# Performance work log

Measured on AMD Instinct MI355X. Metric: run time of the kernel, lower is better.

The kernel has to match this reference:

```python
import jax, jax.numpy as jnp
import numpy as np

H = 32  # hidden_layer_size

def setup_inputs() -> dict:
    key = jax.random.key(0)
    ks = jax.random.split(key, 12)
    B, T, I = 4096, 512, 1
    x = jax.random.normal(ks[0], (B, T, I), dtype=jnp.float32)
    # linear_1: input_size -> H
    W1 = jax.random.normal(ks[1], (H, I), dtype=jnp.float32) * (1.0 / np.sqrt(I))
    b1 = jnp.zeros((H,), dtype=jnp.float32)
    # LSTM layer 0 (input H) and layer 1 (input H); torch gate order i,f,g,o
    Wih0 = jax.random.normal(ks[2], (4 * H, H), dtype=jnp.float32) * np.sqrt(2.0 / H)  # kaiming
    Whh0 = jax.random.normal(ks[3], (4 * H, H), dtype=jnp.float32) * (1.0 / np.sqrt(H))
    bih0 = jnp.zeros((4 * H,), dtype=jnp.float32)
    bhh0 = jnp.zeros((4 * H,), dtype=jnp.float32)
    Wih1 = jax.random.normal(ks[4], (4 * H, H), dtype=jnp.float32) * np.sqrt(2.0 / H)
    Whh1 = jax.random.normal(ks[5], (4 * H, H), dtype=jnp.float32) * (1.0 / np.sqrt(H))
    bih1 = jnp.zeros((4 * H,), dtype=jnp.float32)
    bhh1 = jnp.zeros((4 * H,), dtype=jnp.float32)
    # linear_2: num_layers*H -> 1
    W2 = jax.random.normal(ks[6], (1, 2 * H), dtype=jnp.float32) * (1.0 / np.sqrt(2 * H))
    b2 = jnp.zeros((1,), dtype=jnp.float32)
    return {"x": x, "W1": W1, "b1": b1,
            "Wih0": Wih0, "Whh0": Whh0, "bih0": bih0, "bhh0": bhh0,
            "Wih1": Wih1, "Whh1": Whh1, "bih1": bih1, "bhh1": bhh1,
            "W2": W2, "b2": b2}


def _lstm_layer(inp, Wih, Whh, bih, bhh):
    # inp: [B, T, H_in]; returns (ys [B, T, H], h_final [B, H])
    B = inp.shape[0]
    # precompute input-to-gate projections for all timesteps (one big GEMM)
    pre = jnp.einsum('bti,gi->tbg', inp, Wih) + (bih + bhh)  # [T, B, 4H]

    def step(carry, p_t):
        h, c = carry
        z = p_t + h @ Whh.T  # [B, 4H]
        i, f, g, o = jnp.split(z, 4, axis=-1)
        i = jax.nn.sigmoid(i)
        f = jax.nn.sigmoid(f)
        g = jnp.tanh(g)
        o = jax.nn.sigmoid(o)
        c = f * c + i * g
        h = o * jnp.tanh(c)
        return (h, c), h

    h0 = jnp.zeros((B, H), dtype=inp.dtype)
    c0 = jnp.zeros((B, H), dtype=inp.dtype)
    (h_f, _), ys = jax.lax.scan(step, (h0, c0), pre)
    return jnp.transpose(ys, (1, 0, 2)), h_f


def reference(x, W1, b1, Wih0, Whh0, bih0, bhh0, Wih1, Whh1, bih1, bhh1, W2, b2):
    # linear_1 + ReLU
    h = jax.nn.relu(jnp.einsum('bti,oi->bto', x, W1) + b1)  # [B, T, H]
    y0, hf0 = _lstm_layer(h, Wih0, Whh0, bih0, bhh0)
    _, hf1 = _lstm_layer(y0, Wih1, Whh1, bih1, bhh1)
    # h_n.permute(1,0,2).reshape(B, -1) -> concat layer finals along feature dim
    hcat = jnp.concatenate([hf0, hf1], axis=-1)  # [B, 2H]
    # dropout: eval mode (identity)
    preds = hcat @ W2.T + b2  # [B, 1]
    return preds[:, -1]  # [B]
```

## Files before the change

### kernel.cpp

```cpp
#include <hip/hip_runtime.h>

#define HH 32
#define NB 16
#define NT 512
#define TT 512

typedef float f32x4 __attribute__((ext_vector_type(4)));
typedef __bf16 bf16x8 __attribute__((ext_vector_type(8)));
typedef unsigned int u32;
typedef unsigned short u16;
typedef u32 u32x4 __attribute__((ext_vector_type(4)));

#if __has_builtin(__builtin_amdgcn_exp2f)
#define EXP2F(x) __builtin_amdgcn_exp2f(x)
#else
#define EXP2F(x) exp2f(x)
#endif
#if __has_builtin(__builtin_amdgcn_rcpf)
#define RCPF(x) __builtin_amdgcn_rcpf(x)
#else
#define RCPF(x) (1.0f / (x))
#endif

static __device__ __forceinline__ float sigm(float z) {
  return RCPF(1.0f + EXP2F(z * -1.44269504f));
}
static __device__ __forceinline__ float tanh_fast(float z) {
  return __builtin_fmaf(2.0f, RCPF(1.0f + EXP2F(z * -2.88539008f)), -1.0f);
}
static __device__ __forceinline__ f32x4 mfma16(bf16x8 a, bf16x8 b, f32x4 c) {
  return __builtin_amdgcn_mfma_f32_16x16x32_bf16(a, b, c, 0, 0, 0);
}

static __device__ __forceinline__ u32 rne_hi(u32 b) {
  return (b + 0x7FFFu + ((b >> 16) & 1u)) & 0xFFFF0000u;
}
static __device__ __forceinline__ u32 pack_hi16(u32 a, u32 b) {
#if __has_builtin(__builtin_amdgcn_perm)
  return __builtin_amdgcn_perm(a, b, 0x03020706u);
#else
  return (b & 0xFFFF0000u) | (a >> 16);
#endif
}
static __device__ __forceinline__ void split8(const float f[8], bf16x8* hi, bf16x8* lo) {
  u32 r[8];
  float lof[8];
#pragma unroll
  for (int j = 0; j < 8; ++j) {
    u32 b = __builtin_bit_cast(u32, f[j]);
    r[j] = rne_hi(b);
    lof[j] = f[j] - __builtin_bit_cast(float, r[j]);
  }
  u32x4 hw, lw;
#pragma unroll
  for (int i = 0; i < 4; ++i) {
    hw[i] = pack_hi16(r[2 * i], r[2 * i + 1]);
    lw[i] = pack_hi16(__builtin_bit_cast(u32, lof[2 * i]),
                      __builtin_bit_cast(u32, lof[2 * i + 1]));
  }
  *hi = __builtin_bit_cast(bf16x8, hw);
  *lo = __builtin_bit_cast(bf16x8, lw);
}

static __device__ __forceinline__ void load_wfrag(const float* __restrict__ M,
                                                  int tile, int lane,
                                                  bf16x8* hi, bf16x8* lo) {
  const int m = lane & 15;
  const int gi = (m & 3) * HH + 4 * tile + (m >> 2);
  const int k0 = (lane >> 4) * 8;
  const float* p = M + gi * HH + k0;
  float f[8];
#pragma unroll
  for (int e = 0; e < 8; ++e) f[e] = p[e];
  split8(f, hi, lo);
}

static __device__ __forceinline__ void store_h(u16* hiA, u16* loA, int fw, float h) {
  const u32 b = __builtin_bit_cast(u32, h);
  const u32 r = rne_hi(b);
  hiA[fw] = (u16)(r >> 16);
  const float lof = h - __builtin_bit_cast(float, r);
  loA[fw] = (u16)(__builtin_bit_cast(u32, lof) >> 16);
}

__global__ void __launch_bounds__(NT)
lstm_fused_v3(const float* __restrict__ x,
              const float* __restrict__ W1, const float* __restrict__ b1,
              const float* __restrict__ Wih0, const float* __restrict__ Whh0,
              const float* __restrict__ bih0, const float* __restrict__ bhh0,
              const float* __restrict__ Wih1, const float* __restrict__ Whh1,
              const float* __restrict__ bih1, const float* __restrict__ bhh1,
              const float* __restrict__ W2, const float* __restrict__ b2,
              float* __restrict__ out, int T)
{
  __shared__ __align__(16) u16 h0hi[2][NB * HH], h0lo[2][NB * HH];
  __shared__ __align__(16) u16 h1hi[2][NB * HH], h1lo[2][NB * HH];
  __shared__ __align__(16) u16 hxhi[2][NB * HH], hxlo[2][NB * HH];
  __shared__ __align__(16) float xT[TT * NB];

  const int tid  = threadIdx.x;
  const int w    = tid >> 6;
  const int lane = tid & 63;
  const int ub   = lane & 15;
  const int G    = lane >> 4;
  const int uu   = 4 * w + G;
  const int b0   = blockIdx.x * NB;

  bf16x8 whh0h, whh0l, wih0h, wih0l, wih1h, wih1l, whh1h, whh1l;
  load_wfrag(Whh0, w, lane, &whh0h, &whh0l);
  load_wfrag(Wih0, w, lane, &wih0h, &wih0l);
  load_wfrag(Wih1, w, lane, &wih1h, &wih1l);
  load_wfrag(Whh1, w, lane, &whh1h, &whh1l);

  f32x4 B0c, B1c;
#pragma unroll
  for (int q = 0; q < 4; ++q) {
    B0c[q] = bih0[q * HH + uu] + bhh0[q * HH + uu];
    B1c[q] = bih1[q * HH + uu] + bhh1[q * HH + uu];
  }
  const float W1u = W1[uu];
  const float b1u = b1[uu];

  const int fw  = (ub + ((uu >> 3) << 4)) * 8 + (uu & 7);
  const int frd = lane * 8;

  {
    const int row = tid >> 5;
    const int c0i = (tid & 31) * 16;
    if (c0i + 16 <= T) {
      const float* xp = x + (size_t)(b0 + row) * T + c0i;
#pragma unroll
      for (int j = 0; j < 16; j += 4) {
        float4 v = *(const float4*)(xp + j);
        xT[(c0i + j + 0) * NB + row] = v.x;
        xT[(c0i + j + 1) * NB + row] = v.y;
        xT[(c0i + j + 2) * NB + row] = v.z;
        xT[(c0i + j + 3) * NB + row] = v.w;
      }
    }
  }
  h0hi[0][tid] = 0; h0hi[1][tid] = 0; h0lo[0][tid] = 0; h0lo[1][tid] = 0;
  h1hi[0][tid] = 0; h1hi[1][tid] = 0; h1lo[0][tid] = 0; h1lo[1][tid] = 0;
  {
    const float hv = fmaxf(__builtin_fmaf(x[(size_t)(b0 + ub) * T], W1u, b1u), 0.0f);
    const u32 bb = __builtin_bit_cast(u32, hv);
    const u32 rr = rne_hi(bb);
    hxhi[0][fw] = (u16)(rr >> 16);
    const float lf = hv - __builtin_bit_cast(float, rr);
    hxlo[0][fw] = (u16)(__builtin_bit_cast(u32, lf) >> 16);
  }
  float c0 = 0.0f, c1 = 0.0f, h0v = 0.0f, h1v = 0.0f;
  __syncthreads();

#define STEP(kk, WB, DO_L0, DO_L1, DO_HIN)                                   \
  {                                                                          \
    const int RB = (WB) ^ 1;                                                 \
    const bf16x8 a0h = *(const bf16x8*)&h0hi[RB][frd];                       \
    const bf16x8 a0l = *(const bf16x8*)&h0lo[RB][frd];                       \
    bf16x8 a1h, a1l, axh, axl;                                               \
    if (DO_L1) { a1h = *(const bf16x8*)&h1hi[WB][frd];                       \
                 a1l = *(const bf16x8*)&h1lo[WB][frd]; }                     \
    if (DO_L0) { axh = *(const bf16x8*)&hxhi[WB][frd];                       \
                 axl = *(const bf16x8*)&hxlo[WB][frd]; }                     \
    if (DO_HIN) {        \
      const float xv = xT[((kk) + 1) * NB + ub];                             \
      const float hv = fmaxf(__builtin_fmaf(xv, W1u, b1u), 0.0f);            \
      const u32 bb = __builtin_bit_cast(u32, hv);                            \
      const u32 rr = rne_hi(bb);                                             \
      hxhi[RB][fw] = (u16)(rr >> 16);                                        \
      const float lf = hv - __builtin_bit_cast(float, rr);                   \
      hxlo[RB][fw] = (u16)(__builtin_bit_cast(u32, lf) >> 16);               \
    }                                                                        \
    if (DO_L0) {                                                             \
      f32x4 z = B0c;                                                         \
      z = mfma16(whh0h, a0h, z); z = mfma16(whh0h, a0l, z);                  \
      z = mfma16(whh0l, a0h, z);                                             \
      z = mfma16(wih0h, axh, z); z = mfma16(wih0h, axl, z);                  \
      z = mfma16(wih0l, axh, z);                                             \
      const float iv = sigm(z[0]), fv = sigm(z[1]);                          \
      const float gv = tanh_fast(z[2]), ov = sigm(z[3]);                     \
      c0 = __builtin_fmaf(fv, c0, iv * gv);                                  \
      h0v = ov * tanh_fast(c0);                                              \
      store_h(h0hi[WB], h0lo[WB], fw, h0v);                                  \
    }                                                                        \
    if (DO_L1) {                                                             \
      f32x4 z = B1c;                                                         \
      z = mfma16(whh1h, a1h, z); z = mfma16(whh1h, a1l, z);                  \
      z = mfma16(whh1l, a1h, z);                                             \
      z = mfma16(wih1h, a0h, z); z = mfma16(wih1h, a0l, z);                  \
      z = mfma16(wih1l, a0h, z);                                             \
      const float iv = sigm(z[0]), fv = sigm(z[1]);                          \
      const float gv = tanh_fast(z[2]), ov = sigm(z[3]);                     \
      c1 = __builtin_fmaf(fv, c1, iv * gv);                                  \
      h1v = ov * tanh_fast(c1);                                              \
      store_h(h1hi[RB], h1lo[RB], fw, h1v);                                  \
    }                                                                        \
    __syncthreads();                                                         \
  }

  STEP(0, 0, true, false, true);
  for (int kk = 1; kk + 1 < T; kk += 2) {
    STEP(kk, 1, true, true, true);
    STEP(kk + 1, 0, true, true, true);
  }
  STEP(T - 1, 1, true, true, false);
  STEP(T, 0, false, true, false);

#undef STEP

  xT[uu * NB + ub] = __builtin_fmaf(h0v, W2[uu], h1v * W2[HH + uu]);
  __syncthreads();
  if (tid < NB) {
    float acc = b2[0];
#pragma unroll
    for (int u = 0; u < HH; ++u) acc += xT[u * NB + tid];
    out[b0 + tid] = acc;
  }
}

extern "C" void kernel_launch(void* const* d_in, const int* in_sizes, int n_in,
                              void* d_out, int out_size, void* d_ws, size_t ws_size,
                              hipStream_t stream) {
  const float* x    = (const float*)d_in[0];
  const float* W1   = (const float*)d_in[1];
  const float* b1   = (const float*)d_in[2];
  const float* Wih0 = (const float*)d_in[3];
  const float* Whh0 = (const float*)d_in[4];
  const float* bih0 = (const float*)d_in[5];
  const float* bhh0 = (const float*)d_in[6];
  const float* Wih1 = (const float*)d_in[7];
  const float* Whh1 = (const float*)d_in[8];
  const float* bih1 = (const float*)d_in[9];
  const float* bhh1 = (const float*)d_in[10];
  const float* W2   = (const float*)d_in[11];
  const float* b2   = (const float*)d_in[12];

  const int B = out_size;
  const int I = in_sizes[1] / HH;
  const int T = in_sizes[0] / (B * I);
  const int blocks = B / NB;

  lstm_fused_v3<<<blocks, NT, 0, stream>>>(
      x, W1, b1, Wih0, Whh0, bih0, bhh0, Wih1, Whh1, bih1, bhh1, W2, b2,
      (float*)d_out, T);
}
```

Before: 262.9 us.

## Halve batch per block to 8 rows, doubling blocks and merging MFMA halves via DPP

New measurement: 410.2 us. 1.56x slower.

```diff
diff --git a/kernel.cpp b/kernel.cpp
--- a/kernel.cpp
+++ b/kernel.cpp
@@ -1,8 +1,8 @@
 #include <hip/hip_runtime.h>
 
 #define HH 32
-#define NB 16
-#define NT 512
+#define NB 8
+#define NT 256
 #define TT 512
 
 typedef float f32x4 __attribute__((ext_vector_type(4)));
@@ -22,14 +22,29 @@
 #define RCPF(x) (1.0f / (x))
 #endif
 
-static __device__ __forceinline__ float sigm(float z) {
-  return RCPF(1.0f + EXP2F(z * -1.44269504f));
-}
-static __device__ __forceinline__ float tanh_fast(float z) {
-  return __builtin_fmaf(2.0f, RCPF(1.0f + EXP2F(z * -2.88539008f)), -1.0f);
+#define S_SIGM (-1.44269504f)
+#define S_TANH (-2.88539008f)
+
+static __device__ __forceinline__ float sigm_pre(float zp) {
+  return RCPF(1.0f + EXP2F(zp));
+}
+static __device__ __forceinline__ float tanh_pre(float zp) {
+  return __builtin_fmaf(2.0f, RCPF(1.0f + EXP2F(zp)), -1.0f);
 }
 static __device__ __forceinline__ f32x4 mfma16(bf16x8 a, bf16x8 b, f32x4 c) {
   return __builtin_amdgcn_mfma_f32_16x16x32_bf16(a, b, c, 0, 0, 0);
+}
+
+static __device__ __forceinline__ float merge_dpp(float zA, float zB) {
+#if __has_builtin(__builtin_amdgcn_update_dpp)
+  return __builtin_bit_cast(float, __builtin_amdgcn_update_dpp(
+      __builtin_bit_cast(int, zA), __builtin_bit_cast(int, zB),
+      0x118 , 0xF , 0xC , false));
+#else
+  const int lane = threadIdx.x & 63;
+  const float mv = __shfl_up(zB, 8, 16);
+  return (lane & 8) ? mv : zA;
+#endif
 }
 
 static __device__ __forceinline__ u32 rne_hi(u32 b) {
@@ -62,16 +77,19 @@
   *lo = __builtin_bit_cast(bf16x8, lw);
 }
 
+
 static __device__ __forceinline__ void load_wfrag(const float* __restrict__ M,
                                                   int tile, int lane,
                                                   bf16x8* hi, bf16x8* lo) {
   const int m = lane & 15;
-  const int gi = (m & 3) * HH + 4 * tile + (m >> 2);
-  const int k0 = (lane >> 4) * 8;
-  const float* p = M + gi * HH + k0;
+  const int q = m & 3;
+  const int gi = q * HH + 4 * tile + (m >> 2);
+  const int kappa = lane >> 4;
+  const float s = (q == 2) ? S_TANH : S_SIGM;
   float f[8];
 #pragma unroll
-  for (int e = 0; e < 8; ++e) f[e] = p[e];
+  for (int e = 0; e < 8; ++e)
+    f[e] = M[gi * HH + 8 * kappa + 4 * (e & 1) + (e >> 1)] * s;
   split8(f, hi, lo);
 }
 
@@ -84,7 +102,7 @@
 }
 
 __global__ void __launch_bounds__(NT)
-lstm_fused_v3(const float* __restrict__ x,
+lstm_fused_v4(const float* __restrict__ x,
               const float* __restrict__ W1, const float* __restrict__ b1,
               const float* __restrict__ Wih0, const float* __restrict__ Whh0,
               const float* __restrict__ bih0, const float* __restrict__ bhh0,
@@ -93,36 +111,49 @@
               const float* __restrict__ W2, const float* __restrict__ b2,
               float* __restrict__ out, int T)
 {
-  __shared__ __align__(16) u16 h0hi[2][NB * HH], h0lo[2][NB * HH];
-  __shared__ __align__(16) u16 h1hi[2][NB * HH], h1lo[2][NB * HH];
-  __shared__ __align__(16) u16 hxhi[2][NB * HH], hxlo[2][NB * HH];
+  __shared__ __align__(16) u16 h0hi[2][16 * HH], h0lo[2][16 * HH];
+  __shared__ __align__(16) u16 h1hi[2][16 * HH], h1lo[2][16 * HH];
+  __shared__ __align__(16) u16 hxhi[2][16 * HH], hxlo[2][16 * HH];
   __shared__ __align__(16) float xT[TT * NB];
 
   const int tid  = threadIdx.x;
   const int w    = tid >> 6;
   const int lane = tid & 63;
-  const int ub   = lane & 15;
   const int G    = lane >> 4;
-  const int uu   = 4 * w + G;
   const int b0   = blockIdx.x * NB;
 
-  bf16x8 whh0h, whh0l, wih0h, wih0l, wih1h, wih1l, whh1h, whh1l;
-  load_wfrag(Whh0, w, lane, &whh0h, &whh0l);
-  load_wfrag(Wih0, w, lane, &wih0h, &wih0l);
-  load_wfrag(Wih1, w, lane, &wih1h, &wih1l);
-  load_wfrag(Whh1, w, lane, &whh1h, &whh1l);
-
-  f32x4 B0c, B1c;
-#pragma unroll
-  for (int q = 0; q < 4; ++q) {
-    B0c[q] = bih0[q * HH + uu] + bhh0[q * HH + uu];
-    B1c[q] = bih1[q * HH + uu] + bhh1[q * HH + uu];
-  }
-  const float W1u = W1[uu];
-  const float b1u = b1[uu];
-
-  const int fw  = (ub + ((uu >> 3) << 4)) * 8 + (uu & 7);
+  bf16x8 whh0hA, whh0lA, wih0hA, wih0lA, wih1hA, wih1lA, whh1hA, whh1lA;
+  bf16x8 whh0hB, whh0lB, wih0hB, wih0lB, wih1hB, wih1lB, whh1hB, whh1lB;
+  load_wfrag(Whh0, w,     lane, &whh0hA, &whh0lA);
+  load_wfrag(Wih0, w,     lane, &wih0hA, &wih0lA);
+  load_wfrag(Wih1, w,     lane, &wih1hA, &wih1lA);
+  load_wfrag(Whh1, w,     lane, &whh1hA, &whh1lA);
+  load_wfrag(Whh0, w + 4, lane, &whh0hB, &whh0lB);
+  load_wfrag(Wih0, w + 4, lane, &wih0hB, &wih0lB);
+  load_wfrag(Wih1, w + 4, lane, &wih1hB, &wih1lB);
+  load_wfrag(Whh1, w + 4, lane, &whh1hB, &whh1lB);
+
+  f32x4 bias0A, bias0B, bias1A, bias1B;
+  {
+    const int uA = 4 * w + G, uB = 4 * (w + 4) + G;
+#pragma unroll
+    for (int q = 0; q < 4; ++q) {
+      const float s = (q == 2) ? S_TANH : S_SIGM;
+      bias0A[q] = (bih0[q * HH + uA] + bhh0[q * HH + uA]) * s;
+      bias0B[q] = (bih0[q * HH + uB] + bhh0[q * HH + uB]) * s;
+      bias1A[q] = (bih1[q * HH + uA] + bhh1[q * HH + uA]) * s;
+      bias1B[q] = (bih1[q * HH + uB] + bhh1[q * HH + uB]) * s;
+    }
+  }
+  const f32x4 fzero = {0.f, 0.f, 0.f, 0.f};
+
+  const int bq = lane & 7;
+  const int uu = 4 * w + G + 16 * ((lane >> 3) & 1);
+  const int fw  = (bq + 16 * (uu >> 3)) * 8 + 2 * (uu & 3) + ((uu >> 2) & 1);
   const int frd = lane * 8;
+
+  const float W1u = W1[uu], b1u = b1[uu];
+  const float W2a = W2[uu], W2b = W2[HH + uu];
 
   {
     const int row = tid >> 5;
@@ -139,15 +170,20 @@
       }
     }
   }
-  h0hi[0][tid] = 0; h0hi[1][tid] = 0; h0lo[0][tid] = 0; h0lo[1][tid] = 0;
-  h1hi[0][tid] = 0; h1hi[1][tid] = 0; h1lo[0][tid] = 0; h1lo[1][tid] = 0;
   {
-    const float hv = fmaxf(__builtin_fmaf(x[(size_t)(b0 + ub) * T], W1u, b1u), 0.0f);
-    const u32 bb = __builtin_bit_cast(u32, hv);
-    const u32 rr = rne_hi(bb);
-    hxhi[0][fw] = (u16)(rr >> 16);
-    const float lf = hv - __builtin_bit_cast(float, rr);
-    hxlo[0][fw] = (u16)(__builtin_bit_cast(u32, lf) >> 16);
+    u32* z0 = (u32*)h0hi;
+    (void)z0;
+#pragma unroll
+    for (int j = 0; j < 2; ++j) {
+      ((u32*)h0hi[j])[tid] = 0; ((u32*)h0lo[j])[tid] = 0;
+      ((u32*)h1hi[j])[tid] = 0; ((u32*)h1lo[j])[tid] = 0;
+      ((u32*)hxhi[j])[tid] = 0; ((u32*)hxlo[j])[tid] = 0;
+    }
+  }
+  __syncthreads();
+  {
+    const float hv = fmaxf(__builtin_fmaf(x[(size_t)(b0 + bq) * T], W1u, b1u), 0.0f);
+    store_h(hxhi[0], hxlo[0], fw, hv);
   }
   float c0 = 0.0f, c1 = 0.0f, h0v = 0.0f, h1v = 0.0f;
   __syncthreads();
@@ -162,37 +198,55 @@
                  a1l = *(const bf16x8*)&h1lo[WB][frd]; }                     \
     if (DO_L0) { axh = *(const bf16x8*)&hxhi[WB][frd];                       \
                  axl = *(const bf16x8*)&hxlo[WB][frd]; }                     \
-    if (DO_HIN) {        \
-      const float xv = xT[((kk) + 1) * NB + ub];                             \
+    if (DO_HIN) {                 \
+      const float xv = xT[((kk) + 1) * NB + bq];                             \
       const float hv = fmaxf(__builtin_fmaf(xv, W1u, b1u), 0.0f);            \
-      const u32 bb = __builtin_bit_cast(u32, hv);                            \
-      const u32 rr = rne_hi(bb);                                             \
-      hxhi[RB][fw] = (u16)(rr >> 16);                                        \
-      const float lf = hv - __builtin_bit_cast(float, rr);                   \
-      hxlo[RB][fw] = (u16)(__builtin_bit_cast(u32, lf) >> 16);               \
+      store_h(hxhi[RB], hxlo[RB], fw, hv);                                   \
     }                                                                        \
     if (DO_L0) {                                                             \
-      f32x4 z = B0c;                                                         \
-      z = mfma16(whh0h, a0h, z); z = mfma16(whh0h, a0l, z);                  \
-      z = mfma16(whh0l, a0h, z);                                             \
-      z = mfma16(wih0h, axh, z); z = mfma16(wih0h, axl, z);                  \
-      z = mfma16(wih0l, axh, z);                                             \
-      const float iv = sigm(z[0]), fv = sigm(z[1]);                          \
-      const float gv = tanh_fast(z[2]), ov = sigm(z[3]);                     \
+      f32x4 rA = mfma16(whh0hA, a0h, bias0A);                                \
+      rA = mfma16(whh0hA, a0l, rA);                                          \
+      rA = mfma16(whh0lA, a0h, rA);                                          \
+      f32x4 iA = mfma16(wih0hA, axh, fzero);                                 \
+      iA = mfma16(wih0hA, axl, iA);                                          \
+      iA = mfma16(wih0lA, axh, iA);                                          \
+      f32x4 rB = mfma16(whh0hB, a0h, bias0B);                                \
+      rB = mfma16(whh0hB, a0l, rB);                                          \
+      rB = mfma16(whh0lB, a0h, rB);                                          \
+      f32x4 iB = mfma16(wih0hB, axh, fzero);                                 \
+      iB = mfma16(wih0hB, axl, iB);                                          \
+      iB = mfma16(wih0lB, axh, iB);                                          \
+      const f32x4 zA = rA + iA, zB = rB + iB;                                \
+      f32x4 zm;                                                              \
+      zm[0] = merge_dpp(zA[0], zB[0]); zm[1] = merge_dpp(zA[1], zB[1]);      \
+      zm[2] = merge_dpp(zA[2], zB[2]); zm[3] = merge_dpp(zA[3], zB[3]);      \
+      const float iv = sigm_pre(zm[0]), fv = sigm_pre(zm[1]);                \
+      const float gv = tanh_pre(zm[2]), ov = sigm_pre(zm[3]);                \
       c0 = __builtin_fmaf(fv, c0, iv * gv);                                  \
-      h0v = ov * tanh_fast(c0);                                              \
+      h0v = ov * tanh_pre(c0 * S_TANH);                                      \
       store_h(h0hi[WB], h0lo[WB], fw, h0v);                                  \
     }                                                                        \
     if (DO_L1) {                                                             \
-      f32x4 z = B1c;                                                         \
-      z = mfma16(whh1h, a1h, z); z = mfma16(whh1h, a1l, z);                  \
-      z = mfma16(whh1l, a1h, z);                                             \
-      z = mfma16(wih1h, a0h, z); z = mfma16(wih1h, a0l, z);                  \
-      z = mfma16(wih1l, a0h, z);                                             \
-      const float iv = sigm(z[0]), fv = sigm(z[1]);                          \
-      const float gv = tanh_fast(z[2]), ov = sigm(z[3]);                     \
+      f32x4 rA = mfma16(whh1hA, a1h, bias1A);                                \
+      rA = mfma16(whh1hA, a1l, rA);                                          \
+      rA = mfma16(whh1lA, a1h, rA);                                          \
+      f32x4 iA = mfma16(wih1hA, a0h, fzero);                                 \
+      iA = mfma16(wih1hA, a0l, iA);                                          \
+      iA = mfma16(wih1lA, a0h, iA);                                          \
+      f32x4 rB = mfma16(whh1hB, a1h, bias1B);                                \
+      rB = mfma16(whh1hB, a1l, rB);                                          \
+      rB = mfma16(whh1lB, a1h, rB);                                          \
+      f32x4 iB = mfma16(wih1hB, a0h, fzero);                                 \
+      iB = mfma16(wih1hB, a0l, iB);                                          \
+      iB = mfma16(wih1lB, a0h, iB);                                          \
+      const f32x4 zA = rA + iA, zB = rB + iB;                                \
+      f32x4 zm;                                                              \
+      zm[0] = merge_dpp(zA[0], zB[0]); zm[1] = merge_dpp(zA[1], zB[1]);      \
+      zm[2] = merge_dpp(zA[2], zB[2]); zm[3] = merge_dpp(zA[3], zB[3]);      \
+      const float iv = sigm_pre(zm[0]), fv = sigm_pre(zm[1]);                \
+      const float gv = tanh_pre(zm[2]), ov = sigm_pre(zm[3]);                \
       c1 = __builtin_fmaf(fv, c1, iv * gv);                                  \
-      h1v = ov * tanh_fast(c1);                                              \
+      h1v = ov * tanh_pre(c1 * S_TANH);                                      \
       store_h(h1hi[RB], h1lo[RB], fw, h1v);                                  \
     }                                                                        \
     __syncthreads();                                                         \
@@ -208,7 +262,7 @@
 
 #undef STEP
 
-  xT[uu * NB + ub] = __builtin_fmaf(h0v, W2[uu], h1v * W2[HH + uu]);
+  xT[uu * NB + bq] = __builtin_fmaf(h0v, W2a, h1v * W2b);
   __syncthreads();
   if (tid < NB) {
     float acc = b2[0];
@@ -240,7 +294,7 @@
   const int T = in_sizes[0] / (B * I);
   const int blocks = B / NB;
 
-  lstm_fused_v3<<<blocks, NT, 0, stream>>>(
+  lstm_fused_v4<<<blocks, NT, 0, stream>>>(
       x, W1, b1, Wih0, Whh0, bih0, bhh0, Wih1, Whh1, bih1, bhh1, W2, b2,
       (float*)d_out, T);
 }
```

## Split LSTM layers across wave groups, fold gate scales into weights, drop weight lo-split

Applied to the files above, without the earlier changes.

New measurement: 233.4 us. 1.13x faster.

```diff
diff --git a/kernel.cpp b/kernel.cpp
--- a/kernel.cpp
+++ b/kernel.cpp
@@ -2,7 +2,7 @@
 
 #define HH 32
 #define NB 16
-#define NT 512
+#define NT 1024
 #define TT 512
 
 typedef float f32x4 __attribute__((ext_vector_type(4)));
@@ -22,12 +22,9 @@
 #define RCPF(x) (1.0f / (x))
 #endif
 
-static __device__ __forceinline__ float sigm(float z) {
-  return RCPF(1.0f + EXP2F(z * -1.44269504f));
-}
-static __device__ __forceinline__ float tanh_fast(float z) {
-  return __builtin_fmaf(2.0f, RCPF(1.0f + EXP2F(z * -2.88539008f)), -1.0f);
-}
+#define S_SIGM (-1.44269504f)
+#define S_TANH (-2.88539008f)
+
 static __device__ __forceinline__ f32x4 mfma16(bf16x8 a, bf16x8 b, f32x4 c) {
   return __builtin_amdgcn_mfma_f32_16x16x32_bf16(a, b, c, 0, 0, 0);
 }
@@ -42,37 +39,25 @@
   return (b & 0xFFFF0000u) | (a >> 16);
 #endif
 }
-static __device__ __forceinline__ void split8(const float f[8], bf16x8* hi, bf16x8* lo) {
+
+
+static __device__ __forceinline__ bf16x8 load_wfrag_hi(const float* __restrict__ M,
+                                                       int tile, int lane) {
+  const int m = lane & 15;
+  const int q = m & 3;
+  const int gi = q * HH + 4 * tile + (m >> 2);
+  const int kappa = lane >> 4;
+  const float s = (q == 2) ? S_TANH : S_SIGM;
   u32 r[8];
-  float lof[8];
-#pragma unroll
-  for (int j = 0; j < 8; ++j) {
-    u32 b = __builtin_bit_cast(u32, f[j]);
-    r[j] = rne_hi(b);
-    lof[j] = f[j] - __builtin_bit_cast(float, r[j]);
-  }
-  u32x4 hw, lw;
-#pragma unroll
-  for (int i = 0; i < 4; ++i) {
-    hw[i] = pack_hi16(r[2 * i], r[2 * i + 1]);
-    lw[i] = pack_hi16(__builtin_bit_cast(u32, lof[2 * i]),
-                      __builtin_bit_cast(u32, lof[2 * i + 1]));
-  }
-  *hi = __builtin_bit_cast(bf16x8, hw);
-  *lo = __builtin_bit_cast(bf16x8, lw);
-}
-
-static __device__ __forceinline__ void load_wfrag(const float* __restrict__ M,
-                                                  int tile, int lane,
-                                                  bf16x8* hi, bf16x8* lo) {
-  const int m = lane & 15;
-  const int gi = (m & 3) * HH + 4 * tile + (m >> 2);
-  const int k0 = (lane >> 4) * 8;
-  const float* p = M + gi * HH + k0;
-  float f[8];
-#pragma unroll
-  for (int e = 0; e < 8; ++e) f[e] = p[e];
-  split8(f, hi, lo);
+#pragma unroll
+  for (int e = 0; e < 8; ++e) {
+    const float v = M[gi * HH + 8 * kappa + 4 * (e & 1) + (e >> 1)] * s;
+    r[e] = rne_hi(__builtin_bit_cast(u32, v));
+  }
+  u32x4 hw;
+#pragma unroll
+  for (int i = 0; i < 4; ++i) hw[i] = pack_hi16(r[2 * i], r[2 * i + 1]);
+  return __builtin_bit_cast(bf16x8, hw);
 }
 
 static __device__ __forceinline__ void store_h(u16* hiA, u16* loA, int fw, float h) {
@@ -84,7 +69,7 @@
 }
 
 __global__ void __launch_bounds__(NT)
-lstm_fused_v3(const float* __restrict__ x,
+lstm_fused_v5(const float* __restrict__ x,
               const float* __restrict__ W1, const float* __restrict__ b1,
               const float* __restrict__ Wih0, const float* __restrict__ Whh0,
               const float* __restrict__ bih0, const float* __restrict__ bhh0,
@@ -99,103 +84,112 @@
   __shared__ __align__(16) float xT[TT * NB];
 
   const int tid  = threadIdx.x;
-  const int w    = tid >> 6;
   const int lane = tid & 63;
-  const int ub   = lane & 15;
+  const int wS   = __builtin_amdgcn_readfirstlane(tid >> 6);
+  const bool isL0 = (wS < 8);
+  const int tau  = wS & 7;
   const int G    = lane >> 4;
-  const int uu   = 4 * w + G;
   const int b0   = blockIdx.x * NB;
 
-  bf16x8 whh0h, whh0l, wih0h, wih0l, wih1h, wih1l, whh1h, whh1l;
-  load_wfrag(Whh0, w, lane, &whh0h, &whh0l);
-  load_wfrag(Wih0, w, lane, &wih0h, &wih0l);
-  load_wfrag(Wih1, w, lane, &wih1h, &wih1l);
-  load_wfrag(Whh1, w, lane, &whh1h, &whh1l);
-
-  f32x4 B0c, B1c;
+  const float* Wr   = isL0 ? Whh0 : Whh1;
+  const float* Wi_  = isL0 ? Wih0 : Wih1;
+  const float* bihp = isL0 ? bih0 : bih1;
+  const float* bhhp = isL0 ? bhh0 : bhh1;
+
+  const bf16x8 wr = load_wfrag_hi(Wr,  tau, lane);
+  const bf16x8 wi = load_wfrag_hi(Wi_, tau, lane);
+
+  const int uu = 4 * tau + G;
+  const int bq = lane & 15;
+  f32x4 bias;
 #pragma unroll
   for (int q = 0; q < 4; ++q) {
-    B0c[q] = bih0[q * HH + uu] + bhh0[q * HH + uu];
-    B1c[q] = bih1[q * HH + uu] + bhh1[q * HH + uu];
-  }
-  const float W1u = W1[uu];
-  const float b1u = b1[uu];
-
-  const int fw  = (ub + ((uu >> 3) << 4)) * 8 + (uu & 7);
+    const float s = (q == 2) ? S_TANH : S_SIGM;
+    bias[q] = (bihp[q * HH + uu] + bhhp[q * HH + uu]) * s;
+  }
+  const int fw  = (bq + 16 * (uu >> 3)) * 8 + 2 * (uu & 3) + ((uu >> 2) & 1);
   const int frd = lane * 8;
 
+  const float W1u = W1[uu], b1u = b1[uu];
+  const float W2v = W2[(isL0 ? 0 : HH) + uu];
+
   {
-    const int row = tid >> 5;
-    const int c0i = (tid & 31) * 16;
-    if (c0i + 16 <= T) {
+    const int row = tid & 15;
+    const int c0i = (tid >> 4) * 8;
+    if (c0i + 8 <= T) {
       const float* xp = x + (size_t)(b0 + row) * T + c0i;
-#pragma unroll
-      for (int j = 0; j < 16; j += 4) {
-        float4 v = *(const float4*)(xp + j);
-        xT[(c0i + j + 0) * NB + row] = v.x;
-        xT[(c0i + j + 1) * NB + row] = v.y;
-        xT[(c0i + j + 2) * NB + row] = v.z;
-        xT[(c0i + j + 3) * NB + row] = v.w;
-      }
+      const float4 v0 = *(const float4*)(xp);
+      const float4 v1 = *(const float4*)(xp + 4);
+      xT[(c0i + 0) * NB + row] = v0.x;
+      xT[(c0i + 1) * NB + row] = v0.y;
+      xT[(c0i + 2) * NB + row] = v0.z;
+      xT[(c0i + 3) * NB + row] = v0.w;
+      xT[(c0i + 4) * NB + row] = v1.x;
+      xT[(c0i + 5) * NB + row] = v1.y;
+      xT[(c0i + 6) * NB + row] = v1.z;
+      xT[(c0i + 7) * NB + row] = v1.w;
     }
   }
-  h0hi[0][tid] = 0; h0hi[1][tid] = 0; h0lo[0][tid] = 0; h0lo[1][tid] = 0;
-  h1hi[0][tid] = 0; h1hi[1][tid] = 0; h1lo[0][tid] = 0; h1lo[1][tid] = 0;
-  {
-    const float hv = fmaxf(__builtin_fmaf(x[(size_t)(b0 + ub) * T], W1u, b1u), 0.0f);
-    const u32 bb = __builtin_bit_cast(u32, hv);
-    const u32 rr = rne_hi(bb);
-    hxhi[0][fw] = (u16)(rr >> 16);
-    const float lf = hv - __builtin_bit_cast(float, rr);
-    hxlo[0][fw] = (u16)(__builtin_bit_cast(u32, lf) >> 16);
-  }
-  float c0 = 0.0f, c1 = 0.0f, h0v = 0.0f, h1v = 0.0f;
+  if (tid < 512) {
+    ((u32*)h0hi)[tid] = 0; ((u32*)h0lo)[tid] = 0;
+    ((u32*)h1hi)[tid] = 0; ((u32*)h1lo)[tid] = 0;
+    ((u32*)hxhi)[tid] = 0; ((u32*)hxlo)[tid] = 0;
+  }
   __syncthreads();
-
-#define STEP(kk, WB, DO_L0, DO_L1, DO_HIN)                                   \
-  {                                                                          \
-    const int RB = (WB) ^ 1;                                                 \
-    const bf16x8 a0h = *(const bf16x8*)&h0hi[RB][frd];                       \
-    const bf16x8 a0l = *(const bf16x8*)&h0lo[RB][frd];                       \
-    bf16x8 a1h, a1l, axh, axl;                                               \
-    if (DO_L1) { a1h = *(const bf16x8*)&h1hi[WB][frd];                       \
-                 a1l = *(const bf16x8*)&h1lo[WB][frd]; }                     \
-    if (DO_L0) { axh = *(const bf16x8*)&hxhi[WB][frd];                       \
-                 axl = *(const bf16x8*)&hxlo[WB][frd]; }                     \
-    if (DO_HIN) {        \
-      const float xv = xT[((kk) + 1) * NB + ub];                             \
-      const float hv = fmaxf(__builtin_fmaf(xv, W1u, b1u), 0.0f);            \
-      const u32 bb = __builtin_bit_cast(u32, hv);                            \
-      const u32 rr = rne_hi(bb);                                             \
-      hxhi[RB][fw] = (u16)(rr >> 16);                                        \
-      const float lf = hv - __builtin_bit_cast(float, rr);                   \
-      hxlo[RB][fw] = (u16)(__builtin_bit_cast(u32, lf) >> 16);               \
-    }                                                                        \
-    if (DO_L0) {                                                             \
-      f32x4 z = B0c;                                                         \
-      z = mfma16(whh0h, a0h, z); z = mfma16(whh0h, a0l, z);                  \
-      z = mfma16(whh0l, a0h, z);                                             \
-      z = mfma16(wih0h, axh, z); z = mfma16(wih0h, axl, z);                  \
-      z = mfma16(wih0l, axh, z);                                             \
-      const float iv = sigm(z[0]), fv = sigm(z[1]);                          \
-      const float gv = tanh_fast(z[2]), ov = sigm(z[3]);                     \
-      c0 = __builtin_fmaf(fv, c0, iv * gv);                                  \
-      h0v = ov * tanh_fast(c0);                                              \
-      store_h(h0hi[WB], h0lo[WB], fw, h0v);                                  \
-    }                                                                        \
-    if (DO_L1) {                                                             \
-      f32x4 z = B1c;                                                         \
-      z = mfma16(whh1h, a1h, z); z = mfma16(whh1h, a1l, z);                  \
-      z = mfma16(whh1l, a1h, z);                                             \
-      z = mfma16(wih1h, a0h, z); z = mfma16(wih1h, a0l, z);                  \
-      z = mfma16(wih1l, a0h, z);                                             \
-      const float iv = sigm(z[0]), fv = sigm(z[1]);                          \
-      const float gv = tanh_fast(z[2]), ov = sigm(z[3]);                     \
-      c1 = __builtin_fmaf(fv, c1, iv * gv);                                  \
-      h1v = ov * tanh_fast(c1);                                              \
-      store_h(h1hi[RB], h1lo[RB], fw, h1v);                                  \
-    }                                                                        \
-    __syncthreads();                                                         \
+  if (isL0) {
+    const float hv = fmaxf(__builtin_fmaf(x[(size_t)(b0 + bq) * T], W1u, b1u), 0.0f);
+    store_h(hxhi[0], hxlo[0], fw, hv);
+  }
+  float cS = 0.0f, hS = 0.0f;
+  __syncthreads();
+
+#define GATES(z)                                                        \
+    { const float ei = EXP2F(z[0]), ef = EXP2F(z[1]);                   \
+      const float eg = EXP2F(z[2]), eo = EXP2F(z[3]);                   \
+      const float iv = RCPF(1.0f + ei), fv = RCPF(1.0f + ef);           \
+      const float gv = __builtin_fmaf(2.0f, RCPF(1.0f + eg), -1.0f);    \
+      const float ov = RCPF(1.0f + eo);                                 \
+      cS = __builtin_fmaf(fv, cS, iv * gv);                             \
+      const float th = __builtin_fmaf(2.0f,                             \
+          RCPF(1.0f + EXP2F(cS * S_TANH)), -1.0f);                      \
+      hS = ov * th; }
+
+#define STEP(kk, WB, DO_L0, DO_L1, DO_HIN)                              \
+  {                                                                     \
+    const int RB = (WB) ^ 1;                                            \
+    if (isL0) {                                                         \
+      if (DO_L0) {                                                      \
+        const bf16x8 shi = *(const bf16x8*)&h0hi[RB][frd];              \
+        const bf16x8 slo = *(const bf16x8*)&h0lo[RB][frd];              \
+        const bf16x8 phi = *(const bf16x8*)&hxhi[WB][frd];              \
+        const bf16x8 plo = *(const bf16x8*)&hxlo[WB][frd];              \
+        f32x4 z = mfma16(wi, plo, bias);                                \
+        z = mfma16(wi, phi, z);                                         \
+        z = mfma16(wr, slo, z);                                         \
+        z = mfma16(wr, shi, z);                                         \
+        if (DO_HIN) {                                                   \
+          const float xv = xT[((kk) + 1) * NB + bq];                    \
+          const float hv = fmaxf(__builtin_fmaf(xv, W1u, b1u), 0.0f);   \
+          store_h(hxhi[RB], hxlo[RB], fw, hv);                          \
+        }                                                               \
+        GATES(z);                                                       \
+        store_h(h0hi[WB], h0lo[WB], fw, hS);                            \
+      }                                                                 \
+    } else {                                                            \
+      if (DO_L1) {                                                      \
+        const bf16x8 shi = *(const bf16x8*)&h1hi[WB][frd];              \
+        const bf16x8 slo = *(const bf16x8*)&h1lo[WB][frd];              \
+        const bf16x8 phi = *(const bf16x8*)&h0hi[RB][frd];              \
+        const bf16x8 plo = *(const bf16x8*)&h0lo[RB][frd];              \
+        f32x4 z = mfma16(wi, plo, bias);                                \
+        z = mfma16(wi, phi, z);                                         \
+        z = mfma16(wr, slo, z);                                         \
+        z = mfma16(wr, shi, z);                                         \
+        GATES(z);                                                       \
+        store_h(h1hi[RB], h1lo[RB], fw, hS);                            \
+      }                                                                 \
+    }                                                                   \
+    __syncthreads();                                                    \
   }
 
   STEP(0, 0, true, false, true);
@@ -207,13 +201,14 @@
   STEP(T, 0, false, true, false);
 
 #undef STEP
-
-  xT[uu * NB + ub] = __builtin_fmaf(h0v, W2[uu], h1v * W2[HH + uu]);
+#undef GATES
+
+  xT[((isL0 ? 0 : HH) + uu) * NB + bq] = hS * W2v;
   __syncthreads();
   if (tid < NB) {
     float acc = b2[0];
 #pragma unroll
-    for (int u = 0; u < HH; ++u) acc += xT[u * NB + tid];
+    for (int j = 0; j < 2 * HH; ++j) acc += xT[j * NB + tid];
     out[b0 + tid] = acc;
   }
 }
@@ -240,7 +235,7 @@
   const int T = in_sizes[0] / (B * I);
   const int blocks = B / NB;
 
-  lstm_fused_v3<<<blocks, NT, 0, stream>>>(
+  lstm_fused_v5<<<blocks, NT, 0, stream>>>(
       x, W1, b1, Wih0, Whh0, bih0, bhh0, Wih1, Whh1, bih1, bhh1, W2, b2,
       (float*)d_out, T);
 }
```
